# Kernel optimization log

Hardware: AMD Instinct MI355X
Metric: run time of the kernel (lower is better)

## Reference

```python
import jax, jax.numpy as jnp
import numpy as np

EPS = 1e-8
NEG_INF = -9e15  # matches torch masked_fill value


def setup_inputs() -> dict:
    key = jax.random.key(0)
    k1, k2 = jax.random.split(key)
    B, D = 4096, 512
    p1 = jax.random.normal(k1, (B, D), dtype=jnp.float32)
    p2 = jax.random.normal(k2, (B, D), dtype=jnp.float32)
    return {"p1": p1, "p2": p2}


def reference(p1, p2):
    # NT-Xent / InfoNCE loss as in SimCLR_MODEL.contrastive_loss (temperature = 1).
    z = jnp.concatenate([p1, p2], axis=0)              # [N, D], N = 2B
    # cosine similarity == GEMM of L2-normalized rows (torch eps clamp = 1e-8)
    zn = z / jnp.maximum(jnp.linalg.norm(z, axis=-1, keepdims=True), EPS)
    sim = zn @ zn.T                                     # [N, N]
    N = sim.shape[0]
    idx = jnp.arange(N)
    sim = sim.at[idx, idx].set(NEG_INF)                 # mask self-similarity
    # positive pair of row i is row (i + N/2) mod N (eye rolled by N/2)
    pos = sim[idx, (idx + N // 2) % N]                  # [N]
    nll = -pos + jax.nn.logsumexp(sim, axis=-1)
    return jnp.mean(nll)
```

## Files before the change

kernel.cpp:

```cpp
#include <hip/hip_runtime.h>
#include <hip/hip_bf16.h>
#include <math.h>

#define N_TOT 8192
#define HALF_N 4096
#define D_DIM 512
#define BM 128
#define BK 64
#define NKIT (D_DIM / BK)
#define NTILES 2080

#define WAIT_VM4 0xF74
#define WAIT_VM0 0xF70

typedef float f32x4_t __attribute__((ext_vector_type(4)));
typedef long long i64x2 __attribute__((ext_vector_type(2)));

typedef __attribute__((address_space(1))) unsigned int g_u32;
typedef __attribute__((address_space(3))) unsigned int l_u32;

__global__ __launch_bounds__(256) void k_normalize(
    const float* __restrict__ p1, const float* __restrict__ p2,
    unsigned char* __restrict__ zf8, float* __restrict__ rowsum,
    float* __restrict__ out)
{
    const int w = threadIdx.x >> 6;
    const int lane = threadIdx.x & 63;
    const int row = blockIdx.x * 4 + w;

    if (threadIdx.x < 4) rowsum[blockIdx.x * 4 + threadIdx.x] = 0.0f;
    if (blockIdx.x == 0 && threadIdx.x == 0) out[0] = 0.0f;

    const float* src = (row < HALF_N) ? p1 + (size_t)row * D_DIM
                                      : p2 + (size_t)(row - HALF_N) * D_DIM;
    float4 a = *(const float4*)(src + lane * 4);
    float4 b = *(const float4*)(src + 256 + lane * 4);
    float s = a.x*a.x + a.y*a.y + a.z*a.z + a.w*a.w
            + b.x*b.x + b.y*b.y + b.z*b.z + b.w*b.w;
    #pragma unroll
    for (int m = 1; m < 64; m <<= 1) s += __shfl_xor(s, m, 64);
    float inv = 1.0f / fmaxf(sqrtf(s), 1e-8f);

    int pk0 = __builtin_amdgcn_cvt_pk_fp8_f32(a.x * inv, a.y * inv, 0, false);
    pk0     = __builtin_amdgcn_cvt_pk_fp8_f32(a.z * inv, a.w * inv, pk0, true);
    int pk1 = __builtin_amdgcn_cvt_pk_fp8_f32(b.x * inv, b.y * inv, 0, false);
    pk1     = __builtin_amdgcn_cvt_pk_fp8_f32(b.z * inv, b.w * inv, pk1, true);

    unsigned char* dst = zf8 + (size_t)row * D_DIM;
    const int o0 = lane * 4;
    const int o1 = 256 + lane * 4;
    const int d0 = (o0 & ~63) + ((o0 >> 3) & 3) * 16 + ((o0 >> 5) & 1) * 8 + (o0 & 4);
    const int d1 = (o1 & ~63) + ((o1 >> 3) & 3) * 16 + ((o1 >> 5) & 1) * 8 + (o1 & 4);
    *(int*)(dst + d0) = pk0;
    *(int*)(dst + d1) = pk1;
}

__global__ __launch_bounds__(256, 4) void k_gemm(
    const unsigned char* __restrict__ zf8,
    float* __restrict__ rowsum, float* __restrict__ pos)
{
    __shared__ __align__(16) unsigned char As[3][BM * BK];
    __shared__ __align__(16) unsigned char Bs[3][BM * BK];

    const int tid = threadIdx.x;
    const int lane = tid & 63;
    const int w = tid >> 6;
    const int wr = w >> 1, wc = w & 1;
    const int q = lane >> 4, l15 = lane & 15;

    const int t = blockIdx.x;
    int bi = (int)((sqrtf(8.0f * (float)t + 1.0f) - 1.0f) * 0.5f);
    while ((bi + 1) * (bi + 2) / 2 <= t) ++bi;
    while (bi * (bi + 1) / 2 > t) --bi;
    const int bx = bi;
    const int by = t - bi * (bi + 1) / 2;
    const bool isDiag = (bx == by);
    const bool hasPos = (bx - by == 32);
    const int rowBase = by * BM;
    const int colBase = bx * BM;

    const int ci0 = tid;
    const int ci1 = 256 + tid;
    const int r0 = ci0 >> 2, cc0 = ci0 & 3;
    const int r1 = ci1 >> 2, cc1 = ci1 & 3;
    const int gc0 = cc0 ^ ((r0 >> 1) & 3);
    const int gc1 = cc1 ^ ((r1 >> 1) & 3);

    const unsigned char* gA0 = zf8 + (size_t)(rowBase + r0) * D_DIM + gc0 * 16;
    const unsigned char* gA1 = zf8 + (size_t)(rowBase + r1) * D_DIM + gc1 * 16;
    const unsigned char* gB0 = zf8 + (size_t)(colBase + r0) * D_DIM + gc0 * 16;
    const unsigned char* gB1 = zf8 + (size_t)(colBase + r1) * D_DIM + gc1 * 16;

    auto stage = [&](int buf, int kblk) {
        const int kb = kblk * BK;
        __builtin_amdgcn_global_load_lds((const g_u32*)(gA0 + kb), (l_u32*)&As[buf][ci0 * 16], 16, 0, 0);
        __builtin_amdgcn_global_load_lds((const g_u32*)(gA1 + kb), (l_u32*)&As[buf][ci1 * 16], 16, 0, 0);
        __builtin_amdgcn_global_load_lds((const g_u32*)(gB0 + kb), (l_u32*)&Bs[buf][ci0 * 16], 16, 0, 0);
        __builtin_amdgcn_global_load_lds((const g_u32*)(gB1 + kb), (l_u32*)&Bs[buf][ci1 * 16], 16, 0, 0);
    };

    f32x4_t acc[4][4] = {};

    stage(0, 0);
    stage(1, 1);

    #pragma unroll
    for (int it = 0; it < NKIT; it++) {
        const int cur = it % 3;
        if (it + 1 < NKIT) __builtin_amdgcn_s_waitcnt(WAIT_VM4);
        else               __builtin_amdgcn_s_waitcnt(WAIT_VM0);
        __builtin_amdgcn_s_barrier();

        if (it + 2 < NKIT) stage((it + 2) % 3, it + 2);

        i64x2 aF[4], bF[4];
        #pragma unroll
        for (int i = 0; i < 4; i++) {
            const int ra = wr * 64 + i * 16 + l15;
            const int rb = wc * 64 + i * 16 + l15;
            aF[i] = *(const i64x2*)&As[cur][ra * BK + (q ^ ((ra >> 1) & 3)) * 16];
            bF[i] = *(const i64x2*)&Bs[cur][rb * BK + (q ^ ((rb >> 1) & 3)) * 16];
        }
        #pragma unroll
        for (int h = 0; h < 2; h++)
            #pragma unroll
            for (int i = 0; i < 4; i++)
                #pragma unroll
                for (int j = 0; j < 4; j++)
                    acc[i][j] = __builtin_amdgcn_mfma_f32_16x16x32_fp8_fp8(
                        aF[i][h], bF[j][h], acc[i][j], 0, 0, 0);
    }

    float colacc[4] = {0.f, 0.f, 0.f, 0.f};
    #pragma unroll
    for (int i = 0; i < 4; i++) {
        #pragma unroll
        for (int r = 0; r < 4; r++) {
            const int row = rowBase + wr * 64 + i * 16 + q * 4 + r;
            float rs = 0.0f;
            #pragma unroll
            for (int j = 0; j < 4; j++) {
                const int col = colBase + wc * 64 + j * 16 + l15;
                const float c = acc[i][j][r];
                float e = __expf(c);
                if (isDiag && col == row) e = 0.0f;
                rs += e;
                colacc[j] += e;
                if (hasPos && col == row + HALF_N) { pos[row] = c; pos[col] = c; }
            }
            rs += __shfl_xor(rs, 1); rs += __shfl_xor(rs, 2);
            rs += __shfl_xor(rs, 4); rs += __shfl_xor(rs, 8);
            if (l15 == 0) atomicAdd(&rowsum[row], rs);
        }
    }
    if (!isDiag) {
        #pragma unroll
        for (int j = 0; j < 4; j++) {
            float cs = colacc[j];
            cs += __shfl_xor(cs, 16);
            cs += __shfl_xor(cs, 32);
            if (q == 0) atomicAdd(&rowsum[colBase + wc * 64 + j * 16 + l15], cs);
        }
    }
}

__global__ __launch_bounds__(256) void k_finalize(
    const float* __restrict__ rowsum, const float* __restrict__ pos,
    float* __restrict__ out)
{
    const int t = threadIdx.x;
    const int i = blockIdx.x * 256 + t;
    float s = logf(rowsum[i]) - pos[i];
    #pragma unroll
    for (int m = 1; m < 64; m <<= 1) s += __shfl_xor(s, m, 64);
    __shared__ float red[4];
    if ((t & 63) == 0) red[t >> 6] = s;
    __syncthreads();
    if (t == 0)
        atomicAdd(out, (red[0] + red[1] + red[2] + red[3]) * (1.0f / (float)N_TOT));
}

extern "C" void kernel_launch(void* const* d_in, const int* in_sizes, int n_in,
                              void* d_out, int out_size, void* d_ws, size_t ws_size,
                              hipStream_t stream) {
    const float* p1 = (const float*)d_in[0];
    const float* p2 = (const float*)d_in[1];

    unsigned char* zf8 = (unsigned char*)d_ws;
    float* rowsum = (float*)((char*)d_ws + (size_t)N_TOT * D_DIM);
    float* pos    = rowsum + N_TOT;
    float* outp   = (float*)d_out;

    k_normalize<<<N_TOT / 4, 256, 0, stream>>>(p1, p2, zf8, rowsum, outp);
    k_gemm<<<NTILES, 256, 0, stream>>>(zf8, rowsum, pos);
    k_finalize<<<N_TOT / 256, 256, 0, stream>>>(rowsum, pos, outp);
}
```

Before: 105.8 us.

## Pair adjacent column tiles per block to share the A-tile load

Each 512-thread block now computes two neighbouring upper-triangular tiles that share the same row block. The A tile is staged into LDS once and used by both halves, with one B tile per half. This cuts global and LDS traffic for A and halves the block count. In exchange, LDS per block grows from 6 to 9 staging buffers, and the last tile in each odd-length row duplicates a computation whose result is then discarded.

Result: slower. 114.3 us (+8.0%).

```diff
diff --git a/kernel.cpp b/kernel.cpp
--- a/kernel.cpp
+++ b/kernel.cpp
@@ -8,9 +8,9 @@
 #define BM 128
 #define BK 64
 #define NKIT (D_DIM / BK)
-#define NTILES 2080
-
-#define WAIT_VM4 0xF74
+#define NPAIR 1056
+
+#define WAIT_VM3 0xF73
 #define WAIT_VM0 0xF70
 
 typedef float f32x4_t __attribute__((ext_vector_type(4)));
@@ -55,49 +55,51 @@
     *(int*)(dst + d1) = pk1;
 }
 
-__global__ __launch_bounds__(256, 4) void k_gemm(
+__global__ __launch_bounds__(512, 4) void k_gemm(
     const unsigned char* __restrict__ zf8,
     float* __restrict__ rowsum, float* __restrict__ pos)
 {
     __shared__ __align__(16) unsigned char As[3][BM * BK];
-    __shared__ __align__(16) unsigned char Bs[3][BM * BK];
+    __shared__ __align__(16) unsigned char Bs[2][3][BM * BK];
 
     const int tid = threadIdx.x;
     const int lane = tid & 63;
     const int w = tid >> 6;
-    const int wr = w >> 1, wc = w & 1;
+    const int tsel = w >> 2;
+    const int ws = w & 3;
+    const int wr = ws >> 1, wc = ws & 1;
     const int q = lane >> 4, l15 = lane & 15;
 
-    const int t = blockIdx.x;
-    int bi = (int)((sqrtf(8.0f * (float)t + 1.0f) - 1.0f) * 0.5f);
-    while ((bi + 1) * (bi + 2) / 2 <= t) ++bi;
-    while (bi * (bi + 1) / 2 > t) --bi;
-    const int bx = bi;
-    const int by = t - bi * (bi + 1) / 2;
-    const bool isDiag = (bx == by);
-    const bool hasPos = (bx - by == 32);
+    int by = 0, rem = blockIdx.x;
+    while (true) {
+        const int np = (65 - by) >> 1;
+        if (rem < np) break;
+        rem -= np; ++by;
+    }
+    const int bx0 = by + 2 * rem;
+    const bool dupPair = (bx0 + 1 > 63);
+    const int bx1 = dupPair ? bx0 : bx0 + 1;
+    const int bxT = tsel ? bx1 : bx0;
+    const bool skip = (dupPair && tsel == 1);
+    const bool isDiag = (bxT == by);
+    const bool hasPos = (bxT - by == 32);
     const int rowBase = by * BM;
-    const int colBase = bx * BM;
-
-    const int ci0 = tid;
-    const int ci1 = 256 + tid;
-    const int r0 = ci0 >> 2, cc0 = ci0 & 3;
-    const int r1 = ci1 >> 2, cc1 = ci1 & 3;
-    const int gc0 = cc0 ^ ((r0 >> 1) & 3);
-    const int gc1 = cc1 ^ ((r1 >> 1) & 3);
-
-    const unsigned char* gA0 = zf8 + (size_t)(rowBase + r0) * D_DIM + gc0 * 16;
-    const unsigned char* gA1 = zf8 + (size_t)(rowBase + r1) * D_DIM + gc1 * 16;
-    const unsigned char* gB0 = zf8 + (size_t)(colBase + r0) * D_DIM + gc0 * 16;
-    const unsigned char* gB1 = zf8 + (size_t)(colBase + r1) * D_DIM + gc1 * 16;
+    const int colBase = bxT * BM;
+
+    const int srow = tid >> 2, scc = tid & 3;
+    const int sgc = scc ^ ((srow >> 1) & 3);
+    const unsigned char* gA  = zf8 + (size_t)(rowBase + srow) * D_DIM + sgc * 16;
+    const unsigned char* gB0 = zf8 + (size_t)(bx0 * BM + srow) * D_DIM + sgc * 16;
+    const unsigned char* gB1 = zf8 + (size_t)(bx1 * BM + srow) * D_DIM + sgc * 16;
 
     auto stage = [&](int buf, int kblk) {
         const int kb = kblk * BK;
-        __builtin_amdgcn_global_load_lds((const g_u32*)(gA0 + kb), (l_u32*)&As[buf][ci0 * 16], 16, 0, 0);
-        __builtin_amdgcn_global_load_lds((const g_u32*)(gA1 + kb), (l_u32*)&As[buf][ci1 * 16], 16, 0, 0);
-        __builtin_amdgcn_global_load_lds((const g_u32*)(gB0 + kb), (l_u32*)&Bs[buf][ci0 * 16], 16, 0, 0);
-        __builtin_amdgcn_global_load_lds((const g_u32*)(gB1 + kb), (l_u32*)&Bs[buf][ci1 * 16], 16, 0, 0);
+        __builtin_amdgcn_global_load_lds((const g_u32*)(gA  + kb), (l_u32*)&As[buf][tid * 16], 16, 0, 0);
+        __builtin_amdgcn_global_load_lds((const g_u32*)(gB0 + kb), (l_u32*)&Bs[0][buf][tid * 16], 16, 0, 0);
+        __builtin_amdgcn_global_load_lds((const g_u32*)(gB1 + kb), (l_u32*)&Bs[1][buf][tid * 16], 16, 0, 0);
     };
+
+    const unsigned char* BsT = &Bs[tsel][0][0];
 
     f32x4_t acc[4][4] = {};
 
@@ -107,7 +109,7 @@
     #pragma unroll
     for (int it = 0; it < NKIT; it++) {
         const int cur = it % 3;
-        if (it + 1 < NKIT) __builtin_amdgcn_s_waitcnt(WAIT_VM4);
+        if (it + 1 < NKIT) __builtin_amdgcn_s_waitcnt(WAIT_VM3);
         else               __builtin_amdgcn_s_waitcnt(WAIT_VM0);
         __builtin_amdgcn_s_barrier();
 
@@ -119,7 +121,7 @@
             const int ra = wr * 64 + i * 16 + l15;
             const int rb = wc * 64 + i * 16 + l15;
             aF[i] = *(const i64x2*)&As[cur][ra * BK + (q ^ ((ra >> 1) & 3)) * 16];
-            bF[i] = *(const i64x2*)&Bs[cur][rb * BK + (q ^ ((rb >> 1) & 3)) * 16];
+            bF[i] = *(const i64x2*)&BsT[cur * (BM * BK) + rb * BK + (q ^ ((rb >> 1) & 3)) * 16];
         }
         #pragma unroll
         for (int h = 0; h < 2; h++)
@@ -130,6 +132,8 @@
                     acc[i][j] = __builtin_amdgcn_mfma_f32_16x16x32_fp8_fp8(
                         aF[i][h], bF[j][h], acc[i][j], 0, 0, 0);
     }
+
+    if (skip) return;
 
     float colacc[4] = {0.f, 0.f, 0.f, 0.f};
     #pragma unroll
@@ -192,6 +196,6 @@
     float* outp   = (float*)d_out;
 
     k_normalize<<<N_TOT / 4, 256, 0, stream>>>(p1, p2, zf8, rowsum, outp);
-    k_gemm<<<NTILES, 256, 0, stream>>>(zf8, rowsum, pos);
+    k_gemm<<<NPAIR, 512, 0, stream>>>(zf8, rowsum, pos);
     k_finalize<<<N_TOT / 256, 256, 0, stream>>>(rowsum, pos, outp);
 }
```
